# Performance work log

Hardware: AMD Instinct MI355X
Metric: run time of the kernel (lower is better)

The kernel has to match this reference:

```python
import jax, jax.numpy as jnp
import numpy as np

NUM_BLOCKS = 8
BLOCK_SIZE = 96  # 768 // 8
CHANNEL_FACTOR = 1
SPARSITY_THRESHOLD = 0.01
SCALE = 0.02


def setup_inputs() -> dict:
    key = jax.random.key(0)
    k_x, k_w1, k_b1, k_w2, k_b2 = jax.random.split(key, 5)
    B, L, D = 8, 4096, 768
    bs, nb, cf = BLOCK_SIZE, NUM_BLOCKS, CHANNEL_FACTOR
    x = jax.random.normal(k_x, (B, L, D), dtype=jnp.float32)
    w1 = SCALE * jax.random.normal(k_w1, (2, nb, bs, bs * cf), dtype=jnp.float32)
    b1 = SCALE * jax.random.normal(k_b1, (2, nb, bs * cf), dtype=jnp.float32)
    w2 = SCALE * jax.random.normal(k_w2, (2, nb, bs * cf, bs), dtype=jnp.float32)
    b2 = SCALE * jax.random.normal(k_b2, (2, nb, bs), dtype=jnp.float32)
    return {"x": x, "w1": w1, "b1": b1, "w2": w2, "b2": b2}


def _softshrink(v, lam):
    return jnp.sign(v) * jnp.maximum(jnp.abs(v) - lam, 0.0)


def reference(x, w1, b1, w2, b2):
    bias = x
    B, L, D = x.shape
    nb = w1.shape[1]
    bs = w1.shape[2]
    num_modes = L // 2 + 1
    # rFFT along sequence dim, ortho norm
    xf = jnp.fft.rfft(x.astype(jnp.float32), axis=1, norm="ortho")
    xf = xf.reshape(B, num_modes, nb, bs)
    xr, xi = jnp.real(xf), jnp.imag(xf)
    # hard_thresholding_fraction == 1 -> all modes kept
    # layer 1: complex block-diagonal matmul + bias + relu (applied to re/im separately)
    o1r = jax.nn.relu(jnp.einsum("blni,nio->blno", xr, w1[0])
                      - jnp.einsum("blni,nio->blno", xi, w1[1]) + b1[0])
    o1i = jax.nn.relu(jnp.einsum("blni,nio->blno", xi, w1[0])
                      + jnp.einsum("blni,nio->blno", xr, w1[1]) + b1[1])
    # layer 2: complex block-diagonal matmul + bias
    o2r = (jnp.einsum("blno,noi->blni", o1r, w2[0])
           - jnp.einsum("blno,noi->blni", o1i, w2[1]) + b2[0])
    o2i = (jnp.einsum("blno,noi->blni", o1i, w2[0])
           + jnp.einsum("blno,noi->blni", o1r, w2[1]) + b2[1])
    # softshrink on real and imag parts independently
    o2r = _softshrink(o2r, SPARSITY_THRESHOLD)
    o2i = _softshrink(o2i, SPARSITY_THRESHOLD)
    xc = (o2r + 1j * o2i).reshape(B, num_modes, D)
    y = jnp.fft.irfft(xc, n=L, axis=1, norm="ortho").astype(x.dtype)
    return y + bias
```

## Files before the change

### kernel.cpp

```cpp
#include <hip/hip_runtime.h>
#include <math.h>

#define B_      8
#define L_      4096
#define D_      768
#define NB_     8
#define BS_     96
#define NMODES  2049
#define KPB     2112
#define PLN     ((size_t)B_ * D_ * KPB)
#define WKS     104
#define ASTR    200

static const double PI_D = 3.14159265358979323846;

typedef __attribute__((ext_vector_type(8))) short short8v;
typedef __attribute__((ext_vector_type(8))) unsigned short ushort8v;
typedef __attribute__((ext_vector_type(4))) unsigned short ushort4v;
typedef __attribute__((ext_vector_type(4))) unsigned int uint4v;
typedef __attribute__((ext_vector_type(4))) float f32x4;

__device__ __forceinline__ unsigned short f2bf(float f) {
  union { float f; unsigned u; } v; v.f = f;
  unsigned r = v.u + 0x7FFF + ((v.u >> 16) & 1);
  return (unsigned short)(r >> 16);
}
__device__ __forceinline__ float bf2f(unsigned short h) {
  union { unsigned u; float f; } v; v.u = ((unsigned)h) << 16;
  return v.f;
}

__device__ __forceinline__ float2 cmulf(float2 a, float2 b) {
  return make_float2(a.x * b.x - a.y * b.y, a.x * b.y + a.y * b.x);
}

__global__ __launch_bounds__(256) void prep_weights(const float* __restrict__ w1,
                                                    const float* __restrict__ w2,
                                                    unsigned short* __restrict__ WTg) {
  __shared__ float t[96][97];
  const int id = blockIdx.x;
  const int layer = id >> 4;
  const int hn = id & 15;
  const int tid = threadIdx.x;
  const float* src = (layer ? w2 : w1) + (size_t)hn * 9216;
  for (int it = tid; it < 9216; it += 256) {
    int i = it / 96, o = it - i * 96;
    t[i][o] = src[it];
  }
  __syncthreads();
  unsigned short* dst = WTg + (size_t)id * (96 * WKS);
  for (int it = tid; it < 96 * WKS; it += 256) {
    int o = it / WKS, k = it - o * WKS;
    dst[it] = f2bf(k < 96 ? t[k][o] : 0.f);
  }
}

__global__ __launch_bounds__(256) void transpose_fwd(const float* __restrict__ in,
                                                     float* __restrict__ out) {
  __shared__ float tile[64][65];
  const int b = blockIdx.z;
  const int d0 = blockIdx.x * 64;
  const int l0 = blockIdx.y * 64;
  const int tx = threadIdx.x & 63;
  const int ty = threadIdx.x >> 6;
  const float* ib = in + (size_t)b * L_ * D_;
  for (int r = ty; r < 64; r += 4)
    tile[r][tx] = ib[(size_t)(l0 + r) * D_ + d0 + tx];
  __syncthreads();
  float* ob = out + (size_t)b * D_ * L_;
  for (int r = ty; r < 64; r += 4)
    ob[(size_t)(d0 + r) * L_ + l0 + tx] = tile[tx][r];
}

__global__ __launch_bounds__(256) void transpose_add(const float* __restrict__ T,
                                                     const float* __restrict__ x,
                                                     float* __restrict__ y) {
  __shared__ float tile[64][65];
  const int b = blockIdx.z;
  const int d0 = blockIdx.x * 64;
  const int l0 = blockIdx.y * 64;
  const int tx = threadIdx.x & 63;
  const int ty = threadIdx.x >> 6;
  const float* Tb = T + (size_t)b * D_ * L_;
  for (int r = ty; r < 64; r += 4)
    tile[r][tx] = Tb[(size_t)(d0 + r) * L_ + l0 + tx];
  __syncthreads();
  const float* xb = x + (size_t)b * L_ * D_;
  float* yb = y + (size_t)b * L_ * D_;
  for (int r = ty; r < 64; r += 4) {
    size_t a = (size_t)(l0 + r) * D_ + d0 + tx;
    yb[a] = xb[a] + tile[tx][r];
  }
}

__global__ __launch_bounds__(256) void fft_fwd(const float* __restrict__ T,
                                               unsigned short* __restrict__ SRb,
                                               unsigned short* __restrict__ SIb) {
  __shared__ float2 Sb[2][2048];
  __shared__ float2 TW[1024];
  const int d = blockIdx.x;
  const int b = blockIdx.y;
  const int tid = threadIdx.x;

  for (int j = tid; j < 1024; j += 256) {
    float s, c;
    sincosf(-(float)j * (float)(PI_D / 1024.0), &s, &c);
    TW[j] = make_float2(c, s);
  }

  const float2* xr = (const float2*)(T + ((size_t)b * D_ + d) * L_);
  for (int n = tid; n < 2048; n += 256)
    Sb[0][n] = xr[n];
  __syncthreads();

  int src = 0;
  for (int m = 1; m <= 1024; m <<= 1) {
    for (int t = tid; t < 1024; t += 256) {
      int hi = t & ~(m - 1);
      float2 c0 = Sb[src][t];
      float2 c1 = Sb[src][t + 1024];
      float2 sum = make_float2(c0.x + c1.x, c0.y + c1.y);
      float2 dif = make_float2(c0.x - c1.x, c0.y - c1.y);
      Sb[src ^ 1][t + hi] = sum;
      Sb[src ^ 1][t + hi + m] = cmulf(TW[hi], dif);
    }
    src ^= 1;
    __syncthreads();
  }

  unsigned short* sr = SRb + ((size_t)b * D_ + d) * KPB;
  unsigned short* si = SIb + ((size_t)b * D_ + d) * KPB;
  for (int k = tid; k <= 2048; k += 256) {
    int ia = k & 2047;
    int ib = (2048 - k) & 2047;
    float2 Za = Sb[src][ia];
    float2 Zb = Sb[src][ib];
    Zb.y = -Zb.y;
    float2 sum = make_float2(0.5f * (Za.x + Zb.x), 0.5f * (Za.y + Zb.y));
    float2 dif = make_float2(0.5f * (Za.x - Zb.x), 0.5f * (Za.y - Zb.y));
    float s, c;
    sincosf(-(float)k * (float)(PI_D / 2048.0), &s, &c);
    float2 t = cmulf(make_float2(c, s), dif);
    sr[k] = f2bf((sum.x + t.y) * 0.015625f);
    si[k] = f2bf((sum.y - t.x) * 0.015625f);
  }
}

__device__ __forceinline__ void do_layer(const short* As, const short* Wt0,
                                         const short* Wt1, int wave, int lane,
                                         f32x4 P[6], f32x4 Q[6], f32x4 R[6],
                                         f32x4 S[6]) {
  const int l15 = lane & 15, kg = lane >> 4;
  const int arow = (wave * 16 + l15) * ASTR;
#pragma unroll
  for (int ks = 0; ks < 3; ++ks) {
    const int ak = ks * 32 + kg * 8;
    short8v axr = *(const short8v*)&As[arow + ak];
    short8v axi = *(const short8v*)&As[arow + 96 + ak];
#pragma unroll
    for (int nf = 0; nf < 6; ++nf) {
      const int brow = (nf * 16 + l15) * WKS + ak;
      short8v bwr = *(const short8v*)&Wt0[brow];
      short8v bwi = *(const short8v*)&Wt1[brow];
      P[nf] = __builtin_amdgcn_mfma_f32_16x16x32_bf16(axr, bwr, P[nf], 0, 0, 0);
      Q[nf] = __builtin_amdgcn_mfma_f32_16x16x32_bf16(axi, bwi, Q[nf], 0, 0, 0);
      R[nf] = __builtin_amdgcn_mfma_f32_16x16x32_bf16(axi, bwr, R[nf], 0, 0, 0);
      S[nf] = __builtin_amdgcn_mfma_f32_16x16x32_bf16(axr, bwi, S[nf], 0, 0, 0);
    }
  }
}

__global__ __launch_bounds__(256) void mlp(unsigned short* __restrict__ SRb,
                                           unsigned short* __restrict__ SIb,
                                           const unsigned short* __restrict__ WTg,
                                           const float* __restrict__ b1,
                                           const float* __restrict__ b2) {
  __shared__ short As[13824];
  __shared__ short Wt[2][96 * WKS];
  const int t0 = blockIdx.x, n = blockIdx.y, b = blockIdx.z;
  const int tid = threadIdx.x;
  const int k0 = t0 * 64;
  const int lane = tid & 63, wave = tid >> 6;
  const int l15 = lane & 15, kg = lane >> 4;
  const size_t rowbase = ((size_t)b * D_ + n * BS_) * KPB + k0;

  for (int it = tid; it < 1536; it += 256) {
    int ch = it >> 3, ck = it & 7;
    int chm = (ch < 96) ? ch : ch - 96;
    const unsigned short* src =
        ((ch < 96) ? SRb : SIb) + rowbase + (size_t)chm * KPB + ck * 8;
    ushort8v v = *(const ushort8v*)src;
    int base = (ck * 8) * ASTR + ch;
#pragma unroll
    for (int j = 0; j < 8; ++j) As[base + j * ASTR] = (short)v[j];
  }
  {
    const unsigned short* wr = WTg + (size_t)(0 * 16 + 0 * 8 + n) * (96 * WKS);
    const unsigned short* wi = WTg + (size_t)(0 * 16 + 1 * 8 + n) * (96 * WKS);
    for (int it = tid; it < 2496; it += 256) {
      int m = it / 1248;
      int off = (it - m * 1248) * 8;
      *(uint4v*)&Wt[m][off] = *(const uint4v*)((m ? wi : wr) + off);
    }
  }
  __syncthreads();

  f32x4 P[6], Q[6], R[6], S[6];
#pragma unroll
  for (int nf = 0; nf < 6; ++nf) {
    P[nf] = (f32x4){0.f, 0.f, 0.f, 0.f};
    Q[nf] = (f32x4){0.f, 0.f, 0.f, 0.f};
    R[nf] = (f32x4){0.f, 0.f, 0.f, 0.f};
    S[nf] = (f32x4){0.f, 0.f, 0.f, 0.f};
  }
  do_layer(As, Wt[0], Wt[1], wave, lane, P, Q, R, S);

  f32x4 vr[6], vi[6];
#pragma unroll
  for (int nf = 0; nf < 6; ++nf) {
    int col = nf * 16 + l15;
    float br = b1[(size_t)(0 * NB_ + n) * 96 + col];
    float bi = b1[(size_t)(1 * NB_ + n) * 96 + col];
    vr[nf] = P[nf] - Q[nf];
    vi[nf] = R[nf] + S[nf];
#pragma unroll
    for (int j = 0; j < 4; ++j) {
      vr[nf][j] = fmaxf(vr[nf][j] + br, 0.f);
      vi[nf][j] = fmaxf(vi[nf][j] + bi, 0.f);
    }
  }
  __syncthreads();

  const int mbase = wave * 16 + kg * 4;
#pragma unroll
  for (int nf = 0; nf < 6; ++nf) {
    int col = nf * 16 + l15;
#pragma unroll
    for (int j = 0; j < 4; ++j) {
      As[(mbase + j) * ASTR + col] = (short)f2bf(vr[nf][j]);
      As[(mbase + j) * ASTR + 96 + col] = (short)f2bf(vi[nf][j]);
    }
  }
  {
    const unsigned short* wr = WTg + (size_t)(1 * 16 + 0 * 8 + n) * (96 * WKS);
    const unsigned short* wi = WTg + (size_t)(1 * 16 + 1 * 8 + n) * (96 * WKS);
    for (int it = tid; it < 2496; it += 256) {
      int m = it / 1248;
      int off = (it - m * 1248) * 8;
      *(uint4v*)&Wt[m][off] = *(const uint4v*)((m ? wi : wr) + off);
    }
  }
  __syncthreads();

#pragma unroll
  for (int nf = 0; nf < 6; ++nf) {
    P[nf] = (f32x4){0.f, 0.f, 0.f, 0.f};
    Q[nf] = (f32x4){0.f, 0.f, 0.f, 0.f};
    R[nf] = (f32x4){0.f, 0.f, 0.f, 0.f};
    S[nf] = (f32x4){0.f, 0.f, 0.f, 0.f};
  }
  do_layer(As, Wt[0], Wt[1], wave, lane, P, Q, R, S);

#pragma unroll
  for (int nf = 0; nf < 6; ++nf) {
    int col = nf * 16 + l15;
    float br = b2[(size_t)(0 * NB_ + n) * 96 + col];
    float bi = b2[(size_t)(1 * NB_ + n) * 96 + col];
    vr[nf] = P[nf] - Q[nf];
    vi[nf] = R[nf] + S[nf];
#pragma unroll
    for (int j = 0; j < 4; ++j) {
      float a = vr[nf][j] + br;
      float t = fabsf(a) - 0.01f;
      vr[nf][j] = (t > 0.f) ? copysignf(t, a) : 0.f;
      a = vi[nf][j] + bi;
      t = fabsf(a) - 0.01f;
      vi[nf][j] = (t > 0.f) ? copysignf(t, a) : 0.f;
    }
  }
  __syncthreads();

#pragma unroll
  for (int nf = 0; nf < 6; ++nf) {
    int col = nf * 16 + l15;
    ushort4v pr, pi;
#pragma unroll
    for (int j = 0; j < 4; ++j) {
      pr[j] = f2bf(vr[nf][j]);
      pi[j] = f2bf(vi[nf][j]);
    }
    *(ushort4v*)&As[col * 72 + mbase] = pr;
    *(ushort4v*)&As[(96 + col) * 72 + mbase] = pi;
  }
  __syncthreads();

  for (int it = tid; it < 1536; it += 256) {
    int ch = it >> 3, ck = it & 7;
    int chm = (ch < 96) ? ch : ch - 96;
    ushort8v v = *(const ushort8v*)&As[ch * 72 + ck * 8];
    unsigned short* dst =
        ((ch < 96) ? SRb : SIb) + rowbase + (size_t)chm * KPB + ck * 8;
    if (k0 + ck * 8 + 7 < NMODES) {
      *(ushort8v*)dst = v;
    } else {
#pragma unroll
      for (int j = 0; j < 8; ++j)
        if (k0 + ck * 8 + j < NMODES) dst[j] = v[j];
    }
  }
}

__global__ __launch_bounds__(256) void fft_inv(const unsigned short* __restrict__ SRb,
                                               const unsigned short* __restrict__ SIb,
                                               float* __restrict__ T) {
  __shared__ float2 Sb[2][2048];
  __shared__ float2 TW[1024];
  const int d = blockIdx.x;
  const int b = blockIdx.y;
  const int tid = threadIdx.x;

  for (int j = tid; j < 1024; j += 256) {
    float s, c;
    sincosf((float)j * (float)(PI_D / 1024.0), &s, &c);
    TW[j] = make_float2(c, s);
  }

  const unsigned short* sr = SRb + ((size_t)b * D_ + d) * KPB;
  const unsigned short* si = SIb + ((size_t)b * D_ + d) * KPB;
  for (int k = tid; k < 2048; k += 256) {
    float2 z;
    if (k == 0) {
      float x0 = bf2f(sr[0]);
      float xm = bf2f(sr[2048]);
      z = make_float2(0.5f * (x0 + xm), 0.5f * (x0 - xm));
    } else {
      float2 Xk = make_float2(bf2f(sr[k]), bf2f(si[k]));
      float2 Xm = make_float2(bf2f(sr[2048 - k]), -bf2f(si[2048 - k]));
      float2 E = make_float2(0.5f * (Xk.x + Xm.x), 0.5f * (Xk.y + Xm.y));
      float2 Dm = make_float2(0.5f * (Xk.x - Xm.x), 0.5f * (Xk.y - Xm.y));
      float s, c;
      sincosf((float)k * (float)(PI_D / 2048.0), &s, &c);
      float2 O = cmulf(make_float2(c, s), Dm);
      z = make_float2(E.x - O.y, E.y + O.x);
    }
    Sb[0][k] = z;
  }
  __syncthreads();

  int src = 0;
  for (int m = 1; m <= 1024; m <<= 1) {
    for (int t = tid; t < 1024; t += 256) {
      int hi = t & ~(m - 1);
      float2 c0 = Sb[src][t];
      float2 c1 = Sb[src][t + 1024];
      float2 sum = make_float2(c0.x + c1.x, c0.y + c1.y);
      float2 dif = make_float2(c0.x - c1.x, c0.y - c1.y);
      Sb[src ^ 1][t + hi] = sum;
      Sb[src ^ 1][t + hi + m] = cmulf(TW[hi], dif);
    }
    src ^= 1;
    __syncthreads();
  }

  float2* tb = (float2*)(T + ((size_t)b * D_ + d) * L_);
  for (int n = tid; n < 2048; n += 256) {
    float2 z = Sb[src][n];
    tb[n] = make_float2(0.03125f * z.x, 0.03125f * z.y);
  }
}

extern "C" void kernel_launch(void* const* d_in, const int* in_sizes, int n_in,
                              void* d_out, int out_size, void* d_ws, size_t ws_size,
                              hipStream_t stream) {
  (void)in_sizes; (void)n_in; (void)out_size; (void)ws_size;
  const float* x = (const float*)d_in[0];
  const float* w1 = (const float*)d_in[1];
  const float* b1 = (const float*)d_in[2];
  const float* w2 = (const float*)d_in[3];
  const float* b2 = (const float*)d_in[4];
  unsigned short* SRb = (unsigned short*)d_ws;
  unsigned short* SIb = SRb + PLN;
  float* T = (float*)(SIb + PLN);
  unsigned short* WTg = (unsigned short*)(T + (size_t)B_ * D_ * L_);
  float* y = (float*)d_out;

  prep_weights<<<32, 256, 0, stream>>>(w1, w2, WTg);
  transpose_fwd<<<dim3(D_ / 64, L_ / 64, B_), 256, 0, stream>>>(x, T);
  fft_fwd<<<dim3(D_, B_), 256, 0, stream>>>(T, SRb, SIb);
  mlp<<<dim3(33, NB_, B_), 256, 0, stream>>>(SRb, SIb, WTg, b1, b2);
  fft_inv<<<dim3(D_, B_), 256, 0, stream>>>(SRb, SIb, T);
  transpose_add<<<dim3(D_ / 64, L_ / 64, B_), 256, 0, stream>>>(T, x, y);
}
```

Baseline: 480.7 us.

## Store transposed intermediates in bf16, radix-4 FFT, swizzled LDS, direct MLP stores

Turns the transposed time-domain buffer T from fp32 into bf16, which halves the traffic of the transpose and FFT kernels. Replaces the radix-2 Stockham FFT with radix-4 stages plus one final radix-2 stage, and pads the shared arrays to cut LDS bank conflicts and the number of barriers. Adds an XOR swizzle to the MLP activation tile, and writes the layer-2 output straight to global memory instead of staging it through LDS. Rounding the input x to bf16 before the FFT and the output before the residual add lowers accuracy.

```diff
diff --git a/kernel.cpp b/kernel.cpp
--- a/kernel.cpp
+++ b/kernel.cpp
@@ -29,9 +29,13 @@
   union { unsigned u; float f; } v; v.u = ((unsigned)h) << 16;
   return v.f;
 }
-
 __device__ __forceinline__ float2 cmulf(float2 a, float2 b) {
   return make_float2(a.x * b.x - a.y * b.y, a.x * b.y + a.y * b.x);
+}
+
+__device__ __forceinline__ int as_addr(int row, int ch) {
+  int c = ch >> 3, o = ch & 7;
+  return row * ASTR + (((c ^ ((row >> 3) & 7)) << 3) + o);
 }
 
 __global__ __launch_bounds__(256) void prep_weights(const float* __restrict__ w1,
@@ -56,8 +60,8 @@
 }
 
 __global__ __launch_bounds__(256) void transpose_fwd(const float* __restrict__ in,
-                                                     float* __restrict__ out) {
-  __shared__ float tile[64][65];
+                                                     unsigned short* __restrict__ out) {
+  __shared__ unsigned short tile[64][65];
   const int b = blockIdx.z;
   const int d0 = blockIdx.x * 64;
   const int l0 = blockIdx.y * 64;
@@ -65,23 +69,23 @@
   const int ty = threadIdx.x >> 6;
   const float* ib = in + (size_t)b * L_ * D_;
   for (int r = ty; r < 64; r += 4)
-    tile[r][tx] = ib[(size_t)(l0 + r) * D_ + d0 + tx];
-  __syncthreads();
-  float* ob = out + (size_t)b * D_ * L_;
+    tile[r][tx] = f2bf(ib[(size_t)(l0 + r) * D_ + d0 + tx]);
+  __syncthreads();
+  unsigned short* ob = out + (size_t)b * D_ * L_;
   for (int r = ty; r < 64; r += 4)
     ob[(size_t)(d0 + r) * L_ + l0 + tx] = tile[tx][r];
 }
 
-__global__ __launch_bounds__(256) void transpose_add(const float* __restrict__ T,
+__global__ __launch_bounds__(256) void transpose_add(const unsigned short* __restrict__ T,
                                                      const float* __restrict__ x,
                                                      float* __restrict__ y) {
-  __shared__ float tile[64][65];
+  __shared__ unsigned short tile[64][65];
   const int b = blockIdx.z;
   const int d0 = blockIdx.x * 64;
   const int l0 = blockIdx.y * 64;
   const int tx = threadIdx.x & 63;
   const int ty = threadIdx.x >> 6;
-  const float* Tb = T + (size_t)b * D_ * L_;
+  const unsigned short* Tb = T + (size_t)b * D_ * L_;
   for (int r = ty; r < 64; r += 4)
     tile[r][tx] = Tb[(size_t)(d0 + r) * L_ + l0 + tx];
   __syncthreads();
@@ -89,14 +93,58 @@
   float* yb = y + (size_t)b * L_ * D_;
   for (int r = ty; r < 64; r += 4) {
     size_t a = (size_t)(l0 + r) * D_ + d0 + tx;
-    yb[a] = xb[a] + tile[tx][r];
-  }
-}
-
-__global__ __launch_bounds__(256) void fft_fwd(const float* __restrict__ T,
+    yb[a] = xb[a] + bf2f(tile[tx][r]);
+  }
+}
+
+#define FPAD(i) ((i) + ((i) >> 4))
+
+template <int SGN>
+__device__ __forceinline__ void fft_stages(float2 (*Sb)[2176],
+                                           const float2* __restrict__ TW,
+                                           int tid, int& src) {
+#pragma unroll
+  for (int s = 0; s < 5; ++s) {
+    const int m = 1 << (2 * s);
+    for (int q = tid; q < 512; q += 256) {
+      int lo = q & (m - 1);
+      int mJ = q - lo;
+      float2 x0 = Sb[src][FPAD(q)];
+      float2 x1 = Sb[src][FPAD(q + 512)];
+      float2 x2 = Sb[src][FPAD(q + 1024)];
+      float2 x3 = Sb[src][FPAD(q + 1536)];
+      float2 a = make_float2(x0.x + x2.x, x0.y + x2.y);
+      float2 bb = make_float2(x0.x - x2.x, x0.y - x2.y);
+      float2 c = make_float2(x1.x + x3.x, x1.y + x3.y);
+      float2 dd = make_float2(x1.x - x3.x, x1.y - x3.y);
+      float2 id = (SGN < 0) ? make_float2(dd.y, -dd.x)
+                            : make_float2(-dd.y, dd.x);
+      float2 w1 = TW[mJ];
+      float2 w2 = TW[2 * mJ];
+      float2 w3 = cmulf(w1, w2);
+      int ob = 4 * mJ + lo;
+      Sb[src ^ 1][FPAD(ob)] = make_float2(a.x + c.x, a.y + c.y);
+      Sb[src ^ 1][FPAD(ob + m)] = cmulf(w1, make_float2(bb.x + id.x, bb.y + id.y));
+      Sb[src ^ 1][FPAD(ob + 2 * m)] = cmulf(w2, make_float2(a.x - c.x, a.y - c.y));
+      Sb[src ^ 1][FPAD(ob + 3 * m)] = cmulf(w3, make_float2(bb.x - id.x, bb.y - id.y));
+    }
+    src ^= 1;
+    __syncthreads();
+  }
+  for (int t = tid; t < 1024; t += 256) {
+    float2 c0 = Sb[src][FPAD(t)];
+    float2 c1 = Sb[src][FPAD(t + 1024)];
+    Sb[src ^ 1][FPAD(t)] = make_float2(c0.x + c1.x, c0.y + c1.y);
+    Sb[src ^ 1][FPAD(t + 1024)] = make_float2(c0.x - c1.x, c0.y - c1.y);
+  }
+  src ^= 1;
+  __syncthreads();
+}
+
+__global__ __launch_bounds__(256) void fft_fwd(const unsigned short* __restrict__ T,
                                                unsigned short* __restrict__ SRb,
                                                unsigned short* __restrict__ SIb) {
-  __shared__ float2 Sb[2][2048];
+  __shared__ float2 Sb[2][2176];
   __shared__ float2 TW[1024];
   const int d = blockIdx.x;
   const int b = blockIdx.y;
@@ -108,33 +156,26 @@
     TW[j] = make_float2(c, s);
   }
 
-  const float2* xr = (const float2*)(T + ((size_t)b * D_ + d) * L_);
-  for (int n = tid; n < 2048; n += 256)
-    Sb[0][n] = xr[n];
+  const ushort8v* tb = (const ushort8v*)(T + ((size_t)b * D_ + d) * L_);
+  for (int it = tid; it < 512; it += 256) {
+    ushort8v v = tb[it];
+    int base = it * 4;
+#pragma unroll
+    for (int c = 0; c < 4; ++c)
+      Sb[0][FPAD(base + c)] = make_float2(bf2f(v[2 * c]), bf2f(v[2 * c + 1]));
+  }
   __syncthreads();
 
   int src = 0;
-  for (int m = 1; m <= 1024; m <<= 1) {
-    for (int t = tid; t < 1024; t += 256) {
-      int hi = t & ~(m - 1);
-      float2 c0 = Sb[src][t];
-      float2 c1 = Sb[src][t + 1024];
-      float2 sum = make_float2(c0.x + c1.x, c0.y + c1.y);
-      float2 dif = make_float2(c0.x - c1.x, c0.y - c1.y);
-      Sb[src ^ 1][t + hi] = sum;
-      Sb[src ^ 1][t + hi + m] = cmulf(TW[hi], dif);
-    }
-    src ^= 1;
-    __syncthreads();
-  }
+  fft_stages<-1>(Sb, TW, tid, src);
 
   unsigned short* sr = SRb + ((size_t)b * D_ + d) * KPB;
   unsigned short* si = SIb + ((size_t)b * D_ + d) * KPB;
   for (int k = tid; k <= 2048; k += 256) {
     int ia = k & 2047;
     int ib = (2048 - k) & 2047;
-    float2 Za = Sb[src][ia];
-    float2 Zb = Sb[src][ib];
+    float2 Za = Sb[src][FPAD(ia)];
+    float2 Zb = Sb[src][FPAD(ib)];
     Zb.y = -Zb.y;
     float2 sum = make_float2(0.5f * (Za.x + Zb.x), 0.5f * (Za.y + Zb.y));
     float2 dif = make_float2(0.5f * (Za.x - Zb.x), 0.5f * (Za.y - Zb.y));
@@ -152,11 +193,13 @@
                                          f32x4 S[6]) {
   const int l15 = lane & 15, kg = lane >> 4;
   const int arow = (wave * 16 + l15) * ASTR;
+  const int r3 = ((wave * 16 + l15) >> 3) & 7;
 #pragma unroll
   for (int ks = 0; ks < 3; ++ks) {
+    const int cr = ks * 4 + kg;
+    short8v axr = *(const short8v*)&As[arow + (((cr ^ r3) << 3))];
+    short8v axi = *(const short8v*)&As[arow + ((((cr + 12) ^ r3) << 3))];
     const int ak = ks * 32 + kg * 8;
-    short8v axr = *(const short8v*)&As[arow + ak];
-    short8v axi = *(const short8v*)&As[arow + 96 + ak];
 #pragma unroll
     for (int nf = 0; nf < 6; ++nf) {
       const int brow = (nf * 16 + l15) * WKS + ak;
@@ -175,7 +218,7 @@
                                            const unsigned short* __restrict__ WTg,
                                            const float* __restrict__ b1,
                                            const float* __restrict__ b2) {
-  __shared__ short As[13824];
+  __shared__ short As[64 * ASTR];
   __shared__ short Wt[2][96 * WKS];
   const int t0 = blockIdx.x, n = blockIdx.y, b = blockIdx.z;
   const int tid = threadIdx.x;
@@ -190,9 +233,8 @@
     const unsigned short* src =
         ((ch < 96) ? SRb : SIb) + rowbase + (size_t)chm * KPB + ck * 8;
     ushort8v v = *(const ushort8v*)src;
-    int base = (ck * 8) * ASTR + ch;
-#pragma unroll
-    for (int j = 0; j < 8; ++j) As[base + j * ASTR] = (short)v[j];
+#pragma unroll
+    for (int j = 0; j < 8; ++j) As[as_addr(ck * 8 + j, ch)] = (short)v[j];
   }
   {
     const unsigned short* wr = WTg + (size_t)(0 * 16 + 0 * 8 + n) * (96 * WKS);
@@ -219,8 +261,8 @@
 #pragma unroll
   for (int nf = 0; nf < 6; ++nf) {
     int col = nf * 16 + l15;
-    float br = b1[(size_t)(0 * NB_ + n) * 96 + col];
-    float bi = b1[(size_t)(1 * NB_ + n) * 96 + col];
+    float br = b1[(size_t)n * 96 + col];
+    float bi = b1[(size_t)(NB_ + n) * 96 + col];
     vr[nf] = P[nf] - Q[nf];
     vi[nf] = R[nf] + S[nf];
 #pragma unroll
@@ -237,8 +279,8 @@
     int col = nf * 16 + l15;
 #pragma unroll
     for (int j = 0; j < 4; ++j) {
-      As[(mbase + j) * ASTR + col] = (short)f2bf(vr[nf][j]);
-      As[(mbase + j) * ASTR + 96 + col] = (short)f2bf(vi[nf][j]);
+      As[as_addr(mbase + j, col)] = (short)f2bf(vr[nf][j]);
+      As[as_addr(mbase + j, 96 + col)] = (short)f2bf(vi[nf][j]);
     }
   }
   {
@@ -261,59 +303,39 @@
   }
   do_layer(As, Wt[0], Wt[1], wave, lane, P, Q, R, S);
 
+  const int mk = k0 + mbase;
 #pragma unroll
   for (int nf = 0; nf < 6; ++nf) {
     int col = nf * 16 + l15;
-    float br = b2[(size_t)(0 * NB_ + n) * 96 + col];
-    float bi = b2[(size_t)(1 * NB_ + n) * 96 + col];
-    vr[nf] = P[nf] - Q[nf];
-    vi[nf] = R[nf] + S[nf];
+    float br = b2[(size_t)n * 96 + col];
+    float bi = b2[(size_t)(NB_ + n) * 96 + col];
+    ushort4v qr, qi;
 #pragma unroll
     for (int j = 0; j < 4; ++j) {
-      float a = vr[nf][j] + br;
+      float a = (P[nf][j] - Q[nf][j]) + br;
       float t = fabsf(a) - 0.01f;
-      vr[nf][j] = (t > 0.f) ? copysignf(t, a) : 0.f;
-      a = vi[nf][j] + bi;
+      qr[j] = f2bf((t > 0.f) ? copysignf(t, a) : 0.f);
+      a = (R[nf][j] + S[nf][j]) + bi;
       t = fabsf(a) - 0.01f;
-      vi[nf][j] = (t > 0.f) ? copysignf(t, a) : 0.f;
-    }
-  }
-  __syncthreads();
-
-#pragma unroll
-  for (int nf = 0; nf < 6; ++nf) {
-    int col = nf * 16 + l15;
-    ushort4v pr, pi;
-#pragma unroll
-    for (int j = 0; j < 4; ++j) {
-      pr[j] = f2bf(vr[nf][j]);
-      pi[j] = f2bf(vi[nf][j]);
-    }
-    *(ushort4v*)&As[col * 72 + mbase] = pr;
-    *(ushort4v*)&As[(96 + col) * 72 + mbase] = pi;
-  }
-  __syncthreads();
-
-  for (int it = tid; it < 1536; it += 256) {
-    int ch = it >> 3, ck = it & 7;
-    int chm = (ch < 96) ? ch : ch - 96;
-    ushort8v v = *(const ushort8v*)&As[ch * 72 + ck * 8];
-    unsigned short* dst =
-        ((ch < 96) ? SRb : SIb) + rowbase + (size_t)chm * KPB + ck * 8;
-    if (k0 + ck * 8 + 7 < NMODES) {
-      *(ushort8v*)dst = v;
+      qi[j] = f2bf((t > 0.f) ? copysignf(t, a) : 0.f);
+    }
+    unsigned short* pr = SRb + rowbase + (size_t)col * KPB + mbase;
+    unsigned short* pi = SIb + rowbase + (size_t)col * KPB + mbase;
+    if (mk + 3 < NMODES) {
+      *(ushort4v*)pr = qr;
+      *(ushort4v*)pi = qi;
     } else {
 #pragma unroll
-      for (int j = 0; j < 8; ++j)
-        if (k0 + ck * 8 + j < NMODES) dst[j] = v[j];
+      for (int j = 0; j < 4; ++j)
+        if (mk + j < NMODES) { pr[j] = qr[j]; pi[j] = qi[j]; }
     }
   }
 }
 
 __global__ __launch_bounds__(256) void fft_inv(const unsigned short* __restrict__ SRb,
                                                const unsigned short* __restrict__ SIb,
-                                               float* __restrict__ T) {
-  __shared__ float2 Sb[2][2048];
+                                               unsigned short* __restrict__ T) {
+  __shared__ float2 Sb[2][2176];
   __shared__ float2 TW[1024];
   const int d = blockIdx.x;
   const int b = blockIdx.y;
@@ -343,29 +365,24 @@
       float2 O = cmulf(make_float2(c, s), Dm);
       z = make_float2(E.x - O.y, E.y + O.x);
     }
-    Sb[0][k] = z;
+    Sb[0][FPAD(k)] = z;
   }
   __syncthreads();
 
   int src = 0;
-  for (int m = 1; m <= 1024; m <<= 1) {
-    for (int t = tid; t < 1024; t += 256) {
-      int hi = t & ~(m - 1);
-      float2 c0 = Sb[src][t];
-      float2 c1 = Sb[src][t + 1024];
-      float2 sum = make_float2(c0.x + c1.x, c0.y + c1.y);
-      float2 dif = make_float2(c0.x - c1.x, c0.y - c1.y);
-      Sb[src ^ 1][t + hi] = sum;
-      Sb[src ^ 1][t + hi + m] = cmulf(TW[hi], dif);
-    }
-    src ^= 1;
-    __syncthreads();
-  }
-
-  float2* tb = (float2*)(T + ((size_t)b * D_ + d) * L_);
-  for (int n = tid; n < 2048; n += 256) {
-    float2 z = Sb[src][n];
-    tb[n] = make_float2(0.03125f * z.x, 0.03125f * z.y);
+  fft_stages<+1>(Sb, TW, tid, src);
+
+  ushort8v* tb = (ushort8v*)(T + ((size_t)b * D_ + d) * L_);
+  for (int it = tid; it < 512; it += 256) {
+    ushort8v v;
+    int base = it * 4;
+#pragma unroll
+    for (int c = 0; c < 4; ++c) {
+      float2 z = Sb[src][FPAD(base + c)];
+      v[2 * c] = f2bf(0.03125f * z.x);
+      v[2 * c + 1] = f2bf(0.03125f * z.y);
+    }
+    tb[it] = v;
   }
 }
 
@@ -380,8 +397,8 @@
   const float* b2 = (const float*)d_in[4];
   unsigned short* SRb = (unsigned short*)d_ws;
   unsigned short* SIb = SRb + PLN;
-  float* T = (float*)(SIb + PLN);
-  unsigned short* WTg = (unsigned short*)(T + (size_t)B_ * D_ * L_);
+  unsigned short* T = SIb + PLN;
+  unsigned short* WTg = T + (size_t)B_ * D_ * L_;
   float* y = (float*)d_out;
 
   prep_weights<<<32, 256, 0, stream>>>(w1, w2, WTg);
```

After: 462.7 us. 1.04x faster.
